# Kernel optimization log

Measured on AMD Instinct MI355X. Metric: run time of the kernel, lower is better.

## Reference

```python
import jax, jax.numpy as jnp
import numpy as np

N_QUBITS = 12
LAYERS = 2
BATCH = 1024


def _apply_1q(state, gate, q):
    # state: [B] + [2]*n (wire 0 = leading qubit axis); gate: [2,2] or [B,2,2]
    axis = 1 + q
    st = jnp.moveaxis(state, axis, -1)
    if gate.ndim == 2:
        st = jnp.einsum('ij,...j->...i', gate, st)
    else:  # batched gate (angle depends on the input sample)
        st = jnp.einsum('bij,b...j->b...i', gate, st)
    return jnp.moveaxis(st, -1, axis)


def _apply_cnot(state, c, t):
    # flip target axis on the control=1 slice
    ca, ta = 1 + c, 1 + t
    a0 = jnp.take(state, 0, axis=ca)
    a1 = jnp.take(state, 1, axis=ca)
    ta2 = ta - 1 if ta > ca else ta
    a1 = jnp.flip(a1, axis=ta2)
    return jnp.stack([a0, a1], axis=ca)


def _rx(a):
    # a: [B] -> gate [B,2,2]
    h = 0.5 * a
    c = jnp.cos(h).astype(jnp.complex64)
    s = (-1j) * jnp.sin(h).astype(jnp.complex64)
    return jnp.stack([jnp.stack([c, s], -1), jnp.stack([s, c], -1)], -2)


def _ry(a):
    h = 0.5 * a
    c = jnp.cos(h).astype(jnp.complex64)
    s = jnp.sin(h).astype(jnp.complex64)
    return jnp.stack([jnp.stack([c, -s], -1), jnp.stack([s, c], -1)], -2)


def _rz(a):
    h = 0.5 * a
    e0 = jnp.exp(-1j * h.astype(jnp.complex64))
    e1 = jnp.exp(1j * h.astype(jnp.complex64))
    z = jnp.zeros_like(e0)
    return jnp.stack([jnp.stack([e0, z], -1), jnp.stack([z, e1], -1)], -2)


def setup_inputs() -> dict:
    key = jax.random.key(0)
    k1, k2 = jax.random.split(key)
    x = jax.random.normal(k1, (BATCH, N_QUBITS), dtype=jnp.float32)
    theta = jax.random.normal(k2, (LAYERS, N_QUBITS, 2), dtype=jnp.float32)
    lam = jnp.ones((LAYERS, N_QUBITS), dtype=jnp.float32)
    return {"x": x, "theta": theta, "lam": lam}


def reference(x, theta, lam):
    B = x.shape[0]
    n = N_QUBITS
    # |0...0> state, batched: [B] + [2]*n
    state = jnp.zeros((B,) + (2,) * n, dtype=jnp.complex64)
    state = state.at[(slice(None),) + (0,) * n].set(1.0)
    for l in range(LAYERS):
        for q in range(n):
            state = _apply_1q(state, _rx(lam[l, q] * x[:, q]), q)
        for q in range(n):
            state = _apply_cnot(state, q, (q + 1) % n)
        for q in range(n):
            state = _apply_1q(state, _ry(theta[l, q, 0]), q)
            state = _apply_1q(state, _rz(theta[l, q, 1]), q)
    probs = state.real ** 2 + state.imag ** 2  # [B] + [2]*n
    zs = []
    for q in range(n):
        axes = tuple(i for i in range(1, n + 1) if i != 1 + q)
        p = jnp.sum(probs, axis=axes)  # [B, 2]
        zs.append(p[:, 0] - p[:, 1])   # <Z_q>
    return jnp.stack(zs, axis=1)  # [B, n_qubits]
```

## Files before the change

### kernel.cpp

```cpp
#include <hip/hip_runtime.h>
#include <math.h>

#define NQ 12
#define TPB 512


__device__ __forceinline__ int sg(int j) {
    return (j & ~15) | ((j ^ (j >> 4) ^ (j >> 8)) & 15);
}

__device__ __forceinline__ float2 pk_mul(float2 a, float2 b) {
    float2 d;
    asm("v_pk_mul_f32 %0, %1, %2" : "=v"(d) : "v"(a), "v"(b));
    return d;
}
__device__ __forceinline__ float2 pk_fma(float2 a, float2 b, float2 c) {
    float2 d;
    asm("v_pk_fma_f32 %0, %1, %2, %3" : "=v"(d) : "v"(a), "v"(b), "v"(c));
    return d;
}

#define FOR_PAIRS3(RB, STMT) do {                                     \
    const int msk_ = 1 << (RB);                                       \
    _Pragma("unroll")                                                 \
    for (int h_ = 0; h_ < 4; ++h_) {                                  \
        const int i0 = ((h_ & ~(msk_ - 1)) << 1) | (h_ & (msk_ - 1)); \
        const int i1 = i0 | msk_;                                     \
        STMT;                                                         \
    } } while (0)

#define J_A(r) (((r) << 9) | t)
#define J_B(r) (((t >> 6) << 9) | ((r) << 6) | (t & 63))
#define J_C(r) (((t >> 3) << 6) | ((r) << 3) | (t & 7))
#define J_D(r) ((t << 3) | (r))

#define LOCAL_X(JS, JD) do {                                          \
    _Pragma("unroll")                                                 \
    for (int r_ = 0; r_ < 8; ++r_) S[sg(JS(r_))] = v[r_];             \
    _Pragma("unroll")                                                 \
    for (int r_ = 0; r_ < 8; ++r_) v[r_] = S[sg(JD(r_))];             \
  } while (0)

#define CROSS_X(JS, JD) do {                                          \
    _Pragma("unroll")                                                 \
    for (int r_ = 0; r_ < 8; ++r_) S[sg(JS(r_))] = v[r_];             \
    __syncthreads();                                                  \
    _Pragma("unroll")                                                 \
    for (int r_ = 0; r_ < 8; ++r_) v[r_] = S[sg(JD(r_))];             \
  } while (0)


#define G_GATE(q, RB) do {                                                  \
        float2 csy = co[24 + (q)], csz = co[36 + (q)];                      \
        float2 cy2  = make_float2(csy.x, csy.x);                            \
        float2 sy2  = make_float2(csy.y, csy.y);                            \
        float2 msy2 = make_float2(-csy.y, -csy.y);                          \
        FOR_PAIRS3(RB, {                                                    \
            float2 n0 = pk_fma(v[i1], msy2, pk_mul(v[i0], cy2));            \
            float2 wv = pk_fma(v[i0], sy2, pk_mul(v[i1], cy2));             \
            v[i0] = n0;                                                     \
            v[i1].x = csz.x * wv.x - csz.y * wv.y;                          \
            v[i1].y = csz.x * wv.y + csz.y * wv.x;                          \
        });                                                                 \
    } while (0)

#define RXB_GATE(q, RB) do {                                                \
        float2 cs = co[12 + (q)];                                           \
        float2 c2  = make_float2(cs.x, cs.x);                               \
        float2 s2  = make_float2(cs.y, cs.y);                               \
        float2 ms2 = make_float2(-cs.y, -cs.y);                             \
        FOR_PAIRS3(RB, {                                                    \
            float2 n0 = pk_fma(v[i1], s2, pk_mul(v[i0], c2));               \
            float2 n1 = pk_fma(v[i0], ms2, pk_mul(v[i1], c2));              \
            v[i0] = n0; v[i1] = n1;                                         \
        });                                                                 \
    } while (0)

#define RY_GATE(q, RB) do {                                                 \
        float2 cs = co[48 + (q)];                                           \
        float2 c2  = make_float2(cs.x, cs.x);                               \
        float2 s2  = make_float2(cs.y, cs.y);                               \
        float2 ms2 = make_float2(-cs.y, -cs.y);                             \
        FOR_PAIRS3(RB, {                                                    \
            float2 n0 = pk_fma(v[i1], ms2, pk_mul(v[i0], c2));              \
            float2 n1 = pk_fma(v[i0], s2, pk_mul(v[i1], c2));               \
            v[i0] = n0; v[i1] = n1;                                         \
        });                                                                 \
    } while (0)

#define G_PHASE(QB)  do { _Pragma("unroll")                                 \
    for (int d_ = 0; d_ < 3; ++d_) G_GATE((QB) + d_, 2 - d_); } while (0)
#define RXB_PHASE(QB) do { _Pragma("unroll")                                \
    for (int d_ = 0; d_ < 3; ++d_) RXB_GATE((QB) + d_, 2 - d_); } while (0)
#define RY_PHASE(QB) do { _Pragma("unroll")                                 \
    for (int d_ = 0; d_ < 3; ++d_) RY_GATE((QB) + d_, 2 - d_); } while (0)

__global__ __launch_bounds__(TPB) void vqc_kernel(
    const float* __restrict__ x,
    const float* __restrict__ th,
    const float* __restrict__ lm,
    float* __restrict__ out)
{
    __shared__ float2 S[4096];
    __shared__ float2 co[60];

    const int b = blockIdx.x;
    const int t = threadIdx.x;
    const int l = t & 63;
    const int w = t >> 6;

    if (t < 60) {
        float h;
        if (t < 12)       h = 0.5f * lm[t] * x[b * NQ + t];
        else if (t < 24)  h = 0.5f * lm[t] * x[b * NQ + (t - 12)];
        else if (t < 36)  h = 0.5f * th[2 * (t - 24)];
        else if (t < 48)  h = th[2 * (t - 36) + 1];
        else              h = 0.5f * th[24 + 2 * (t - 48)];
        float c, s;
        __sincosf(h, &s, &c);
        co[t].x = c; co[t].y = s;
    }
    __syncthreads();

    float2 v[8];

    {
        const int g = (t ^ (t >> 1)) & 0xFF;
        float Pt = 1.0f;
#pragma unroll
        for (int p = 0; p < 8; ++p) {
            float2 cs = co[11 - p];
            Pt *= ((g >> p) & 1) ? cs.y : cs.x;
        }
        const int ct = __popc(g);
        const int t8 = (t >> 8) & 1, t0 = t & 1;
        float2 q3 = co[3], q2 = co[2], q1 = co[1], q0 = co[0];
        const float u3  = t8 ? q3.y : q3.x;
        const float u3n = t8 ? q3.x : q3.y;
        const float u1  = t0 ? q1.y : q1.x;
        const float u1n = t0 ? q1.x : q1.y;
        const float u0  = t0 ? q0.y : q0.x;
        const float u0n = t0 ? q0.x : q0.y;
#pragma unroll
        for (int r = 0; r < 8; ++r) {
            const int r0 = r & 1, r1 = (r >> 1) & 1, r2 = (r >> 2) & 1;
            const int i9 = r0 ^ r1;
            float m = Pt * (r0 ? u3n : u3) * (i9 ? q2.y : q2.x)
                         * ((r1 ^ r2) ? u1n : u1) * (r2 ? u0n : u0);
            int k = (ct + (t8 ^ r0) + i9 + (t0 ^ r1 ^ r2) + (t0 ^ r2)) & 3;
            v[r].x = (k == 0) ? m : ((k == 2) ? -m : 0.0f);
            v[r].y = (k == 3) ? m : ((k == 1) ? -m : 0.0f);
        }
    }

    G_PHASE(0);
    CROSS_X(J_A, J_B);
    G_PHASE(3);
    LOCAL_X(J_B, J_C);
    G_PHASE(6);
    LOCAL_X(J_C, J_D);
    G_PHASE(9);

    {
        const int pct = __popc(t);
#pragma unroll
        for (int r = 0; r < 8; ++r) {
            int k = (pct + __popc(r)) & 3;
            float2 a = v[r];
            float nx = (k & 1) ? a.y : a.x;
            float ny = (k & 1) ? -a.x : a.y;
            v[r].x = (k & 2) ? -nx : nx;
            v[r].y = (k & 2) ? -ny : ny;
        }
    }

    RXB_PHASE(9);
    LOCAL_X(J_D, J_C);
    RXB_PHASE(6);
    LOCAL_X(J_C, J_B);
    RXB_PHASE(3);
    CROSS_X(J_B, J_A);
    RXB_PHASE(0);

    {
        const int pct = __popc(t);
#pragma unroll
        for (int r = 0; r < 8; ++r) {
            int k = (pct + __popc(r)) & 3;
            float2 a = v[r];
            float nx = (k & 1) ? -a.y : a.x;
            float ny = (k & 1) ? a.x : a.y;
            v[r].x = (k & 2) ? -nx : nx;
            v[r].y = (k & 2) ? -ny : ny;
        }
    }

    __syncthreads();
#pragma unroll
    for (int r = 0; r < 8; ++r) {
        int j = J_A(r);
        int y = j ^ (j >> 1); y ^= y >> 2; y ^= y >> 4; y ^= y >> 8;
        int p = (y & 0x7FF) | (((__popc(j) ^ (j >> 11)) & 1) << 11);
        S[sg(p)] = v[r];
    }
    __syncthreads();
#pragma unroll
    for (int r = 0; r < 8; ++r) v[r] = S[sg(J_D(r))];

    RY_PHASE(9);
    LOCAL_X(J_D, J_C);
    RY_PHASE(6);
    LOCAL_X(J_C, J_B);
    RY_PHASE(3);
    CROSS_X(J_B, J_A);
    RY_PHASE(0);

    float ptot = 0.0f;
    float zb[3] = {0.f, 0.f, 0.f};
#pragma unroll
    for (int r = 0; r < 8; ++r) {
        float p = v[r].x * v[r].x + v[r].y * v[r].y;
        ptot += p;
#pragma unroll
        for (int q = 0; q < 3; ++q)
            zb[q] += ((r >> (2 - q)) & 1) ? -p : p;
    }
    float tv[NQ];
#pragma unroll
    for (int q = 0; q < 3; ++q) tv[q] = zb[q];
#pragma unroll
    for (int q = 3; q < 12; ++q)
        tv[q] = ((t >> (11 - q)) & 1) ? -ptot : ptot;

#pragma unroll
    for (int q = 0; q < NQ; ++q) {
#pragma unroll
        for (int m = 1; m < 64; m <<= 1)
            tv[q] += __shfl_xor(tv[q], m, 64);
    }

    __syncthreads();
    float* red = (float*)S;
    if (l == 0) {
#pragma unroll
        for (int q = 0; q < NQ; ++q) red[w * NQ + q] = tv[q];
    }
    __syncthreads();
    if (t < NQ) {
        float r = 0.f;
#pragma unroll
        for (int ww = 0; ww < 8; ++ww) r += red[ww * NQ + t];
        out[b * NQ + t] = r;
    }
}

extern "C" void kernel_launch(void* const* d_in, const int* in_sizes, int n_in,
                              void* d_out, int out_size, void* d_ws, size_t ws_size,
                              hipStream_t stream) {
    const int B = in_sizes[0] / NQ;
    vqc_kernel<<<B, TPB, 0, stream>>>((const float*)d_in[0],
                                      (const float*)d_in[1],
                                      (const float*)d_in[2],
                                      (float*)d_out);
}
```

Measured before the change: 87.06 us.

## Fuse layer-1 RY·RZ·RX gates into one per-qubit unitary and trim passes

Folds the first layer's RY and RZ gates together with the second layer's RX gate into a single precomputed 2x2 unitary per qubit, factored as two phase rotations around a real rotation. This removes a full gate sweep, an extra cross-warp shared-memory exchange and the diagonal phase fix-up loops. The initial product state is re-derived for the new qubit-to-register mapping. The final reduction switches to a butterfly shuffle that computes all Z expectations with fewer shuffles. This adds more setup math per block and relies on the re-derived index and sign bookkeeping being exactly right.

New measurement: 79.76 us. -8.4%, faster.

```diff
diff --git a/kernel.cpp b/kernel.cpp
--- a/kernel.cpp
+++ b/kernel.cpp
@@ -41,43 +41,25 @@
     for (int r_ = 0; r_ < 8; ++r_) v[r_] = S[sg(JD(r_))];             \
   } while (0)
 
-#define CROSS_X(JS, JD) do {                                          \
-    _Pragma("unroll")                                                 \
-    for (int r_ = 0; r_ < 8; ++r_) S[sg(JS(r_))] = v[r_];             \
-    __syncthreads();                                                  \
-    _Pragma("unroll")                                                 \
-    for (int r_ = 0; r_ < 8; ++r_) v[r_] = S[sg(JD(r_))];             \
-  } while (0)
-
-
-#define G_GATE(q, RB) do {                                                  \
-        float2 csy = co[24 + (q)], csz = co[36 + (q)];                      \
-        float2 cy2  = make_float2(csy.x, csy.x);                            \
-        float2 sy2  = make_float2(csy.y, csy.y);                            \
-        float2 msy2 = make_float2(-csy.y, -csy.y);                          \
+#define M_GATE(q, RB) do {                                                  \
+        float4 A4 = mA[q]; float2 P2 = mB[q];                               \
+        float2 c2  = make_float2(A4.x, A4.x);                               \
+        float2 s2  = make_float2(A4.y, A4.y);                               \
+        float2 ms2 = make_float2(-A4.y, -A4.y);                             \
         FOR_PAIRS3(RB, {                                                    \
-            float2 n0 = pk_fma(v[i1], msy2, pk_mul(v[i0], cy2));            \
-            float2 wv = pk_fma(v[i0], sy2, pk_mul(v[i1], cy2));             \
+            float2 a1 = v[i1];                                              \
+            float2 b1 = make_float2(A4.z*a1.x - A4.w*a1.y,                  \
+                                    A4.z*a1.y + A4.w*a1.x);                 \
+            float2 n0 = pk_fma(b1, ms2, pk_mul(v[i0], c2));                 \
+            float2 n1 = pk_fma(v[i0], s2, pk_mul(b1, c2));                  \
             v[i0] = n0;                                                     \
-            v[i1].x = csz.x * wv.x - csz.y * wv.y;                          \
-            v[i1].y = csz.x * wv.y + csz.y * wv.x;                          \
+            v[i1] = make_float2(P2.x*n1.x - P2.y*n1.y,                      \
+                                P2.x*n1.y + P2.y*n1.x);                     \
         });                                                                 \
     } while (0)
 
-#define RXB_GATE(q, RB) do {                                                \
-        float2 cs = co[12 + (q)];                                           \
-        float2 c2  = make_float2(cs.x, cs.x);                               \
-        float2 s2  = make_float2(cs.y, cs.y);                               \
-        float2 ms2 = make_float2(-cs.y, -cs.y);                             \
-        FOR_PAIRS3(RB, {                                                    \
-            float2 n0 = pk_fma(v[i1], s2, pk_mul(v[i0], c2));               \
-            float2 n1 = pk_fma(v[i0], ms2, pk_mul(v[i1], c2));              \
-            v[i0] = n0; v[i1] = n1;                                         \
-        });                                                                 \
-    } while (0)
-
 #define RY_GATE(q, RB) do {                                                 \
-        float2 cs = co[48 + (q)];                                           \
+        float2 cs = coY[q];                                                 \
         float2 c2  = make_float2(cs.x, cs.x);                               \
         float2 s2  = make_float2(cs.y, cs.y);                               \
         float2 ms2 = make_float2(-cs.y, -cs.y);                             \
@@ -88,10 +70,8 @@
         });                                                                 \
     } while (0)
 
-#define G_PHASE(QB)  do { _Pragma("unroll")                                 \
-    for (int d_ = 0; d_ < 3; ++d_) G_GATE((QB) + d_, 2 - d_); } while (0)
-#define RXB_PHASE(QB) do { _Pragma("unroll")                                \
-    for (int d_ = 0; d_ < 3; ++d_) RXB_GATE((QB) + d_, 2 - d_); } while (0)
+#define M_PHASE(QB)  do { _Pragma("unroll")                                 \
+    for (int d_ = 0; d_ < 3; ++d_) M_GATE((QB) + d_, 2 - d_); } while (0)
 #define RY_PHASE(QB) do { _Pragma("unroll")                                 \
     for (int d_ = 0; d_ < 3; ++d_) RY_GATE((QB) + d_, 2 - d_); } while (0)
 
@@ -102,98 +82,95 @@
     float* __restrict__ out)
 {
     __shared__ float2 S[4096];
-    __shared__ float2 co[60];
+    __shared__ float4 mA[12];
+    __shared__ float2 mB[12];
+    __shared__ float2 coI[12];
+    __shared__ float2 coY[12];
+    __shared__ float red[8 * 12];
 
     const int b = blockIdx.x;
     const int t = threadIdx.x;
     const int l = t & 63;
     const int w = t >> 6;
 
-    if (t < 60) {
-        float h;
-        if (t < 12)       h = 0.5f * lm[t] * x[b * NQ + t];
-        else if (t < 24)  h = 0.5f * lm[t] * x[b * NQ + (t - 12)];
-        else if (t < 36)  h = 0.5f * th[2 * (t - 24)];
-        else if (t < 48)  h = th[2 * (t - 36) + 1];
-        else              h = 0.5f * th[24 + 2 * (t - 48)];
-        float c, s;
-        __sincosf(h, &s, &c);
-        co[t].x = c; co[t].y = s;
+    if (t < 12) {
+        float h = 0.5f * lm[t] * x[b * NQ + t];
+        float c, s; __sincosf(h, &s, &c);
+        coI[t] = make_float2(c, s);
+    } else if (t < 24) {
+        int q = t - 12;
+        float h = 0.5f * th[24 + 2 * q];
+        float c, s; __sincosf(h, &s, &c);
+        coY[q] = make_float2(c, s);
+    } else if (t < 36) {
+        int q = t - 24;
+        float ha = 0.5f * lm[12 + q] * x[b * NQ + q];
+        float hy = 0.5f * th[2 * q];
+        float hz = 0.5f * th[2 * q + 1];
+        float ca, sa, cy, sy, cz, sz;
+        __sincosf(ha, &sa, &ca);
+        __sincosf(hy, &sy, &cy);
+        __sincosf(hz, &sz, &cz);
+        float ax = ca*cy*cz + sa*sy*sz;
+        float ay = -(ca*cy*sz + sa*sy*cz);
+        float bx = ca*sy*cz - sa*cy*sz;
+        float by = ca*sy*sz - sa*cy*cz;
+        float na = ax*ax + ay*ay, nb = bx*bx + by*by;
+        float ra = rsqrtf(fmaxf(na, 1e-30f));
+        float rb = rsqrtf(fmaxf(nb, 1e-30f));
+        float ux = ax*ra, uy = ay*ra;
+        float wx = bx*rb, wy = by*rb;
+        mA[q] = make_float4(na*ra, nb*rb,
+                            ux*wx - uy*wy, -(ux*wy + uy*wx));
+        mB[q] = make_float2(ux*wx + uy*wy, ux*wy - uy*wx);
     }
     __syncthreads();
 
     float2 v[8];
 
     {
-        const int g = (t ^ (t >> 1)) & 0xFF;
+        const int g = (t ^ (t >> 1)) & 0x7F;
         float Pt = 1.0f;
 #pragma unroll
-        for (int p = 0; p < 8; ++p) {
-            float2 cs = co[11 - p];
-            Pt *= ((g >> p) & 1) ? cs.y : cs.x;
+        for (int m = 0; m < 7; ++m) {
+            float2 cs = coI[8 - m];
+            Pt *= ((g >> m) & 1) ? cs.y : cs.x;
         }
         const int ct = __popc(g);
-        const int t8 = (t >> 8) & 1, t0 = t & 1;
-        float2 q3 = co[3], q2 = co[2], q1 = co[1], q0 = co[0];
-        const float u3  = t8 ? q3.y : q3.x;
-        const float u3n = t8 ? q3.x : q3.y;
-        const float u1  = t0 ? q1.y : q1.x;
-        const float u1n = t0 ? q1.x : q1.y;
-        const float u0  = t0 ? q0.y : q0.x;
-        const float u0n = t0 ? q0.x : q0.y;
+        const int t0 = t & 1, t8 = (t >> 8) & 1;
+        const int e1 = ((t >> 7) ^ (t >> 8)) & 1;
+        float2 q11 = coI[11], q10 = coI[10], q9 = coI[9],
+               q1 = coI[1], q0 = coI[0];
+        const float u9  = t0 ? q9.y : q9.x;
+        const float u9n = t0 ? q9.x : q9.y;
+        const float u1  = e1 ? q1.y : q1.x;
+        const float u1n = e1 ? q1.x : q1.y;
+        const float u0  = t8 ? q0.y : q0.x;
+        const float u0n = t8 ? q0.x : q0.y;
 #pragma unroll
         for (int r = 0; r < 8; ++r) {
             const int r0 = r & 1, r1 = (r >> 1) & 1, r2 = (r >> 2) & 1;
-            const int i9 = r0 ^ r1;
-            float m = Pt * (r0 ? u3n : u3) * (i9 ? q2.y : q2.x)
-                         * ((r1 ^ r2) ? u1n : u1) * (r2 ? u0n : u0);
-            int k = (ct + (t8 ^ r0) + i9 + (t0 ^ r1 ^ r2) + (t0 ^ r2)) & 3;
+            const int b11 = r0 ^ r1, b10 = r1 ^ r2;
+            float m = Pt * (b11 ? q11.y : q11.x) * (b10 ? q10.y : q10.x)
+                         * (r2 ? u9n : u9) * (r0 ? u1n : u1)
+                         * (r0 ? u0n : u0);
+            int k = (ct + b11 + b10 + (r2 ^ t0) + (r0 ^ e1) + (r0 ^ t8)) & 3;
             v[r].x = (k == 0) ? m : ((k == 2) ? -m : 0.0f);
             v[r].y = (k == 3) ? m : ((k == 1) ? -m : 0.0f);
         }
     }
 
-    G_PHASE(0);
-    CROSS_X(J_A, J_B);
-    G_PHASE(3);
-    LOCAL_X(J_B, J_C);
-    G_PHASE(6);
-    LOCAL_X(J_C, J_D);
-    G_PHASE(9);
-
-    {
-        const int pct = __popc(t);
-#pragma unroll
-        for (int r = 0; r < 8; ++r) {
-            int k = (pct + __popc(r)) & 3;
-            float2 a = v[r];
-            float nx = (k & 1) ? a.y : a.x;
-            float ny = (k & 1) ? -a.x : a.y;
-            v[r].x = (k & 2) ? -nx : nx;
-            v[r].y = (k & 2) ? -ny : ny;
-        }
-    }
-
-    RXB_PHASE(9);
+    M_PHASE(9);
     LOCAL_X(J_D, J_C);
-    RXB_PHASE(6);
+    M_PHASE(6);
     LOCAL_X(J_C, J_B);
-    RXB_PHASE(3);
-    CROSS_X(J_B, J_A);
-    RXB_PHASE(0);
-
-    {
-        const int pct = __popc(t);
-#pragma unroll
-        for (int r = 0; r < 8; ++r) {
-            int k = (pct + __popc(r)) & 3;
-            float2 a = v[r];
-            float nx = (k & 1) ? -a.y : a.x;
-            float ny = (k & 1) ? a.x : a.y;
-            v[r].x = (k & 2) ? -nx : nx;
-            v[r].y = (k & 2) ? -ny : ny;
-        }
-    }
+    M_PHASE(3);
+#pragma unroll
+    for (int r = 0; r < 8; ++r) S[sg(J_B(r))] = v[r];
+    __syncthreads();
+#pragma unroll
+    for (int r = 0; r < 8; ++r) v[r] = S[sg(J_A(r))];
+    M_PHASE(0);
 
     __syncthreads();
 #pragma unroll
@@ -205,52 +182,59 @@
     }
     __syncthreads();
 #pragma unroll
-    for (int r = 0; r < 8; ++r) v[r] = S[sg(J_D(r))];
-
+    for (int r = 0; r < 8; ++r) v[r] = S[sg(J_A(r))];
+
+    RY_PHASE(0);
+    __syncthreads();
+#pragma unroll
+    for (int r = 0; r < 8; ++r) S[sg(J_A(r))] = v[r];
+    __syncthreads();
+#pragma unroll
+    for (int r = 0; r < 8; ++r) v[r] = S[sg(J_B(r))];
+    RY_PHASE(3);
+    LOCAL_X(J_B, J_C);
+    RY_PHASE(6);
+    LOCAL_X(J_C, J_D);
     RY_PHASE(9);
-    LOCAL_X(J_D, J_C);
-    RY_PHASE(6);
-    LOCAL_X(J_C, J_B);
-    RY_PHASE(3);
-    CROSS_X(J_B, J_A);
-    RY_PHASE(0);
-
-    float ptot = 0.0f;
-    float zb[3] = {0.f, 0.f, 0.f};
+
+    float ptot = 0.f, z9 = 0.f, z10 = 0.f, z11 = 0.f;
 #pragma unroll
     for (int r = 0; r < 8; ++r) {
-        float p = v[r].x * v[r].x + v[r].y * v[r].y;
+        float p = fmaf(v[r].x, v[r].x, v[r].y * v[r].y);
         ptot += p;
-#pragma unroll
-        for (int q = 0; q < 3; ++q)
-            zb[q] += ((r >> (2 - q)) & 1) ? -p : p;
-    }
-    float tv[NQ];
-#pragma unroll
-    for (int q = 0; q < 3; ++q) tv[q] = zb[q];
-#pragma unroll
-    for (int q = 3; q < 12; ++q)
-        tv[q] = ((t >> (11 - q)) & 1) ? -ptot : ptot;
-
-#pragma unroll
-    for (int q = 0; q < NQ; ++q) {
-#pragma unroll
-        for (int m = 1; m < 64; m <<= 1)
-            tv[q] += __shfl_xor(tv[q], m, 64);
-    }
-
-    __syncthreads();
-    float* red = (float*)S;
+        z9  += (r & 4) ? -p : p;
+        z10 += (r & 2) ? -p : p;
+        z11 += (r & 1) ? -p : p;
+    }
+    float vals[4] = {ptot, z9, z10, z11};
+#pragma unroll
+    for (int k = 0; k < 6; ++k) {
+        const float sgn = ((l >> k) & 1) ? -1.f : 1.f;
+#pragma unroll
+        for (int m = 0; m < 4; ++m) {
+            float tmp = __shfl_xor(vals[m], 1 << k, 64);
+            vals[m] = fmaf(sgn, vals[m], tmp);
+        }
+    }
     if (l == 0) {
-#pragma unroll
-        for (int q = 0; q < NQ; ++q) red[w * NQ + q] = tv[q];
+        red[w * 12 + 0]  = vals[0];
+        red[w * 12 + 9]  = vals[1];
+        red[w * 12 + 10] = vals[2];
+        red[w * 12 + 11] = vals[3];
+    } else if (__popc(l) == 1) {
+        int q = 9 - __ffs(l);
+        red[w * 12 + q] = vals[0];
     }
     __syncthreads();
     if (t < NQ) {
-        float r = 0.f;
-#pragma unroll
-        for (int ww = 0; ww < 8; ++ww) r += red[ww * NQ + t];
-        out[b * NQ + t] = r;
+        float acc = 0.f;
+#pragma unroll
+        for (int ww = 0; ww < 8; ++ww) {
+            float vv = red[ww * 12 + (t < 3 ? 0 : t)];
+            if (t < 3) acc += ((ww >> (2 - t)) & 1) ? -vv : vv;
+            else       acc += vv;
+        }
+        out[b * NQ + t] = acc;
     }
 }
 
```
